# Kernel tuning notes

Measured on AMD Instinct MI355X. Metric: run time of the kernel, lower is better.

Reference implementation:

```python
import jax, jax.numpy as jnp
import numpy as np

D_MODEL = 128
NUM_HEADS = 4
HEAD_DIM = D_MODEL // NUM_HEADS  # 32
SCALE = 1.0 / np.sqrt(HEAD_DIM)
LAMBDA_INIT = 0.8
EPS = 1e-5


def _layernorm(x, w, b):
    mu = jnp.mean(x, axis=-1, keepdims=True)
    var = jnp.var(x, axis=-1, keepdims=True)
    return (x - mu) * jax.lax.rsqrt(var + EPS) * w + b


def setup_inputs() -> dict:
    key = jax.random.key(0)
    ks = jax.random.split(key, 10)
    B, T, D = 8, 2048, D_MODEL
    inp = {
        "tokens": jax.random.normal(ks[0], (B, T, D), dtype=jnp.float32),
        "ln_w": jnp.ones((D,), jnp.float32),
        "ln_b": jnp.zeros((D,), jnp.float32),
        "wq": jax.random.normal(ks[1], (D, 2 * D), jnp.float32) * (1.0 / np.sqrt(D)),
        "wk": jax.random.normal(ks[2], (D, 2 * D), jnp.float32) * (1.0 / np.sqrt(D)),
        "wv": jax.random.normal(ks[3], (D, 2 * D), jnp.float32) * (1.0 / np.sqrt(D)),
        "wo": jax.random.normal(ks[4], (2 * D, D), jnp.float32) * (1.0 / np.sqrt(2 * D)),
        "lambda_q1": jax.random.normal(ks[5], (HEAD_DIM,), jnp.float32) * 0.1,
        "lambda_k1": jax.random.normal(ks[6], (HEAD_DIM,), jnp.float32) * 0.1,
        "lambda_q2": jax.random.normal(ks[7], (HEAD_DIM,), jnp.float32) * 0.1,
        "lambda_k2": jax.random.normal(ks[8], (HEAD_DIM,), jnp.float32) * 0.1,
        "sigma_signal": jnp.asarray(3.0, jnp.float32),
        "sigma_noise": jnp.asarray(10.0, jnp.float32),
        "hn_w": jnp.ones((2 * HEAD_DIM,), jnp.float32),
        "hn_b": jnp.zeros((2 * HEAD_DIM,), jnp.float32),
    }
    return inp


def reference(tokens, ln_w, ln_b, wq, wk, wv, wo,
              lambda_q1, lambda_k1, lambda_q2, lambda_k2,
              sigma_signal, sigma_noise, hn_w, hn_b):
    B, T, D = tokens.shape
    H, hd = NUM_HEADS, HEAD_DIM

    x = _layernorm(tokens, ln_w, ln_b)

    def heads(x, w):  # [B,T,D] @ [D,2D] -> [B,H,T,2*hd]
        return (x @ w).reshape(B, T, H, 2 * hd).transpose(0, 2, 1, 3)

    q = heads(x, wq)
    k = heads(x, wk)
    v = heads(x, wv)
    q1, q2 = q[..., :hd], q[..., hd:]
    k1, k2 = k[..., :hd], k[..., hd:]

    scores1 = jnp.einsum('bhqd,bhkd->bhqk', q1, k1) * SCALE
    scores2 = jnp.einsum('bhqd,bhkd->bhqk', q2, k2) * SCALE

    # temporal Gaussian bias, shared sigma mode: [T,T] broadcast over [B,H]
    pos = jnp.arange(T, dtype=tokens.dtype)
    rel = pos[None, :] - pos[:, None]  # rel_dist[i,j] = j - i
    sig_s = jnp.maximum(sigma_signal, 1.0)
    sig_n = jnp.maximum(sigma_noise, 1.0)
    scores1 = scores1 + (-0.5 * (rel / sig_s) ** 2)
    scores2 = scores2 + (-0.5 * (rel / sig_n) ** 2)

    attn1 = jax.nn.softmax(scores1, axis=-1)
    attn2 = jax.nn.softmax(scores2, axis=-1)

    lam = jnp.exp(jnp.dot(lambda_q1, lambda_k1)) - jnp.exp(jnp.dot(lambda_q2, lambda_k2)) + LAMBDA_INIT

    out = jnp.einsum('bhqk,bhkd->bhqd', attn1 - lam * attn2, v)  # [B,H,T,2*hd]
    out = _layernorm(out, hn_w, hn_b)
    out = out * (1.0 - LAMBDA_INIT)
    out = out.transpose(0, 2, 1, 3).reshape(B, T, 2 * D)
    out = out @ wo
    return tokens + out
```

## Files before the change

### kernel.cpp

```cpp
#include <hip/hip_runtime.h>
#include <hip/hip_bf16.h>

#define TSEQ 2048
#define BATCH 8
#define NHEAD 4
#define BH (BATCH*NHEAD)
#define HD 32
#define SCALE 0.17677669529663687f
#define LAMBDA_INIT 0.8f
#define LN_EPS 1e-5f

typedef __attribute__((ext_vector_type(8))) short short8;
typedef __attribute__((ext_vector_type(4))) float f32x4;

static __device__ __forceinline__ unsigned short f2bf(float x) {
    unsigned int u = __float_as_uint(x);
    unsigned int r = (u + 0x7fffu + ((u >> 16) & 1u)) >> 16;
    return (unsigned short)r;
}

__global__ __launch_bounds__(256) void k_prep(
    const float* __restrict__ wq, const float* __restrict__ wk,
    const float* __restrict__ wv, const float* __restrict__ wo,
    unsigned short* __restrict__ WqkvT, unsigned short* __restrict__ WoT)
{
    __shared__ float xt[64][65];
    const int bid = blockIdx.x, tid = threadIdx.x;
    const float* src; int srcN, k0, nsrc0, dstK;
    unsigned short* dst;
    if (bid < 24) {
        int ntile = bid >> 1, ktile = bid & 1;
        int gn0 = ntile * 64; k0 = ktile * 64;
        int mat = gn0 >> 8;
        src = (mat == 0) ? wq : (mat == 1 ? wk : wv);
        srcN = 256; nsrc0 = gn0 & 255;
        dst = WqkvT + (size_t)gn0 * 128; dstK = 128;
    } else {
        int b2 = bid - 24;
        int ntile = b2 >> 2, ktile = b2 & 3;
        int gn0 = ntile * 64; k0 = ktile * 64;
        src = wo; srcN = 128; nsrc0 = gn0;
        dst = WoT + (size_t)gn0 * 256; dstK = 256;
    }
    {
        int r = tid >> 2, cs = tid & 3;
        const float* sp = src + (size_t)(k0 + r) * srcN + nsrc0 + cs * 16;
        #pragma unroll
        for (int j = 0; j < 4; j++) {
            float4 v = *(const float4*)(sp + j * 4);
            xt[r][cs * 16 + j * 4 + 0] = v.x;
            xt[r][cs * 16 + j * 4 + 1] = v.y;
            xt[r][cs * 16 + j * 4 + 2] = v.z;
            xt[r][cs * 16 + j * 4 + 3] = v.w;
        }
    }
    __syncthreads();
    {
        int n = tid >> 2, ks = tid & 3;
        short8 o0, o1;
        #pragma unroll
        for (int j = 0; j < 8; j++) {
            o0[j] = (short)f2bf(xt[ks * 16 + j][n]);
            o1[j] = (short)f2bf(xt[ks * 16 + 8 + j][n]);
        }
        unsigned short* dp = dst + (size_t)n * dstK + k0 + ks * 16;
        *(short8*)dp = o0;
        *(short8*)(dp + 8) = o1;
    }
}

__global__ __launch_bounds__(256) void k_qkv(
    const float* __restrict__ tokens, const float* __restrict__ ln_w,
    const float* __restrict__ ln_b, const unsigned short* __restrict__ WqkvT,
    unsigned short* __restrict__ Qg, unsigned short* __restrict__ Kg,
    unsigned short* __restrict__ Vtg)
{
    __shared__ unsigned short x_lds[32][132];
    __shared__ unsigned short c_lds[4][16][68];
    const int tid = threadIdx.x;
    const int r0 = blockIdx.x * 32;

    {
        int row = tid >> 3, sub = tid & 7;
        const float* tr = tokens + (size_t)(r0 + row) * 128 + sub * 16;
        float v[16]; float s = 0.f, sq = 0.f;
        #pragma unroll
        for (int j = 0; j < 16; j += 4) {
            float4 t4 = *(const float4*)(tr + j);
            v[j] = t4.x; v[j + 1] = t4.y; v[j + 2] = t4.z; v[j + 3] = t4.w;
        }
        #pragma unroll
        for (int j = 0; j < 16; j++) { s += v[j]; sq += v[j] * v[j]; }
        #pragma unroll
        for (int m = 1; m < 8; m <<= 1) { s += __shfl_xor(s, m, 64); sq += __shfl_xor(sq, m, 64); }
        float mean = s * (1.f / 128.f);
        float var  = sq * (1.f / 128.f) - mean * mean;
        float rstd = rsqrtf(var + LN_EPS);
        short8 o0, o1;
        #pragma unroll
        for (int j = 0; j < 8; j++) {
            int c0 = sub * 16 + j, c1 = sub * 16 + 8 + j;
            o0[j] = (short)f2bf((v[j] - mean) * rstd * ln_w[c0] + ln_b[c0]);
            o1[j] = (short)f2bf((v[8 + j] - mean) * rstd * ln_w[c1] + ln_b[c1]);
        }
        *(short8*)&x_lds[row][sub * 16] = o0;
        *(short8*)&x_lds[row][sub * 16 + 8] = o1;
    }
    __syncthreads();

    const int w = tid >> 6, lane = tid & 63;
    const int lg = lane >> 4, li = lane & 15;
    const int rt = w >> 1, ch = w & 1;

    short8 a[4];
    #pragma unroll
    for (int kc = 0; kc < 4; kc++)
        a[kc] = *(const short8*)&x_lds[rt * 16 + li][kc * 32 + lg * 8];

    const int b   = r0 >> 11;
    const int tw0 = (r0 & 2047) + rt * 16;

    #pragma unroll
    for (int cc = 0; cc < 6; cc++) {
        f32x4 acc[4] = {};
        #pragma unroll
        for (int t = 0; t < 4; t++) {
            int n0 = ch * 384 + cc * 64 + t * 16;
            const unsigned short* bp = WqkvT + (size_t)(n0 + li) * 128 + lg * 8;
            #pragma unroll
            for (int kc = 0; kc < 4; kc++) {
                short8 bf = *(const short8*)(bp + kc * 32);
                acc[t] = __builtin_amdgcn_mfma_f32_16x16x32_bf16(a[kc], bf, acc[t], 0, 0, 0);
            }
        }
        #pragma unroll
        for (int t = 0; t < 4; t++)
            #pragma unroll
            for (int r = 0; r < 4; r++)
                c_lds[w][lg * 4 + r][t * 16 + li] = f2bf(acc[t][r]);

        int gc = ch * 6 + cc;
        int kind = gc >> 2, h = gc & 3;
        size_t bhh = (size_t)(b * NHEAD + h);
        if (kind < 2) {
            unsigned short* base = (kind == 0) ? Qg : Kg;
            int row = lane >> 2, seg = lane & 3;
            unsigned short* dp = base + (bhh * TSEQ + tw0 + row) * 64 + seg * 16;
            *(short8*)dp       = *(const short8*)&c_lds[w][row][seg * 16];
            *(short8*)(dp + 8) = *(const short8*)&c_lds[w][row][seg * 16 + 8];
        } else {
            int d = lane;
            short8 v0, v1;
            #pragma unroll
            for (int j = 0; j < 8; j++) {
                v0[j] = (short)c_lds[w][j][d];
                v1[j] = (short)c_lds[w][8 + j][d];
            }
            unsigned short* dp = Vtg + (bhh * 64 + d) * TSEQ + tw0;
            *(short8*)dp = v0;
            *(short8*)(dp + 8) = v1;
        }
    }
}

__global__ __launch_bounds__(64) void k_attn(
    const unsigned short* __restrict__ Qg, const unsigned short* __restrict__ Kg,
    const unsigned short* __restrict__ Vtg,
    const float* __restrict__ lq1, const float* __restrict__ lk1,
    const float* __restrict__ lq2, const float* __restrict__ lk2,
    const float* __restrict__ sig_s_p, const float* __restrict__ sig_n_p,
    const float* __restrict__ hn_w, const float* __restrict__ hn_b,
    unsigned short* __restrict__ attn_out)
{
    __shared__ unsigned short p_lds[2][32][36];

    const int lane = threadIdx.x;
    const int lg   = lane >> 4;
    const int li   = lane & 15;

    const int xcd = blockIdx.x & 7;
    const int idx = blockIdx.x >> 3;
    const int bh  = (xcd << 2) | (idx >> 6);
    const int qw  = (idx & 63) * 32;

    float d1 = 0.f, d2 = 0.f;
    for (int i = 0; i < HD; i++) { d1 += lq1[i] * lk1[i]; d2 += lq2[i] * lk2[i]; }
    const float lam = __expf(d1) - __expf(d2) + LAMBDA_INIT;
    const float ss = fmaxf(sig_s_p[0], 1.f);
    const float sn = fmaxf(sig_n_p[0], 1.f);
    const float c1 = -0.5f / (ss * ss);
    const float c2 = -0.5f / (sn * sn);

    int W = (int)ceilf(fmaxf(ss, sn) * 8.f);
    W = (W + 31) & ~31;
    if (W < 64) W = 64;
    int lo = qw - W; if (lo < 0) lo = 0; lo &= ~31;
    int hi = qw + 32 + W; hi = (hi + 31) & ~31; if (hi > TSEQ) hi = TSEQ;

    short8 q1[2], q2[2];
    #pragma unroll
    for (int qt = 0; qt < 2; qt++) {
        const unsigned short* qp = Qg + ((size_t)bh * TSEQ + (qw + qt * 16 + li)) * 64;
        q1[qt] = *(const short8*)(qp + lg * 8);
        q2[qt] = *(const short8*)(qp + 32 + lg * 8);
    }

    const unsigned short* kbase = Kg  + ((size_t)bh * TSEQ + li) * 64 + lg * 8;
    const unsigned short* vbase = Vtg + ((size_t)bh * 64 + li) * TSEQ + lg * 8;

    f32x4 acc1[2][4] = {}, acc2[2][4] = {};
    float ls1[2][4] = {}, ls2[2][4] = {};
    const f32x4 zero4 = {0.f, 0.f, 0.f, 0.f};

    for (int kv = lo; kv < hi; kv += 32) {
        const unsigned short* kp = kbase + (size_t)kv * 64;
        short8 kf1[2], kf2[2];
        kf1[0] = *(const short8*)(kp);
        kf2[0] = *(const short8*)(kp + 32);
        kf1[1] = *(const short8*)(kp + 1024);
        kf2[1] = *(const short8*)(kp + 1024 + 32);

        #pragma unroll
        for (int qt = 0; qt < 2; qt++) {
            f32x4 s1[2], s2[2];
            #pragma unroll
            for (int kt = 0; kt < 2; kt++) {
                s1[kt] = __builtin_amdgcn_mfma_f32_16x16x32_bf16(q1[qt], kf1[kt], zero4, 0, 0, 0);
                s2[kt] = __builtin_amdgcn_mfma_f32_16x16x32_bf16(q2[qt], kf2[kt], zero4, 0, 0, 0);
            }
            const float rb = (float)(kv + li - qw - qt * 16 - 4 * lg);
            #pragma unroll
            for (int kt = 0; kt < 2; kt++) {
                #pragma unroll
                for (int r = 0; r < 4; r++) {
                    float rel = rb + (float)(16 * kt - r);
                    float rr  = rel * rel;
                    float e1  = __expf(fmaf(s1[kt][r], SCALE, c1 * rr));
                    float e2  = __expf(fmaf(s2[kt][r], SCALE, c2 * rr));
                    ls1[qt][r] += e1;
                    ls2[qt][r] += e2;
                    p_lds[0][qt * 16 + lg * 4 + r][kt * 16 + li] = f2bf(e1);
                    p_lds[1][qt * 16 + lg * 4 + r][kt * 16 + li] = f2bf(e2);
                }
            }
        }

        const unsigned short* vp = vbase + kv;
        short8 vf[4];
        #pragma unroll
        for (int dt = 0; dt < 4; dt++)
            vf[dt] = *(const short8*)(vp + (size_t)dt * 16 * TSEQ);

        #pragma unroll
        for (int qt = 0; qt < 2; qt++) {
            short8 pa1 = *(const short8*)&p_lds[0][qt * 16 + li][lg * 8];
            short8 pa2 = *(const short8*)&p_lds[1][qt * 16 + li][lg * 8];
            #pragma unroll
            for (int dt = 0; dt < 4; dt++) {
                acc1[qt][dt] = __builtin_amdgcn_mfma_f32_16x16x32_bf16(pa1, vf[dt], acc1[qt][dt], 0, 0, 0);
                acc2[qt][dt] = __builtin_amdgcn_mfma_f32_16x16x32_bf16(pa2, vf[dt], acc2[qt][dt], 0, 0, 0);
            }
        }
    }

    #pragma unroll
    for (int qt = 0; qt < 2; qt++)
        #pragma unroll
        for (int r = 0; r < 4; r++) {
            #pragma unroll
            for (int m = 1; m < 16; m <<= 1) {
                ls1[qt][r] += __shfl_xor(ls1[qt][r], m, 64);
                ls2[qt][r] += __shfl_xor(ls2[qt][r], m, 64);
            }
        }

    float hw[4], hb[4];
    #pragma unroll
    for (int t = 0; t < 4; t++) { hw[t] = hn_w[t * 16 + li]; hb[t] = hn_b[t * 16 + li]; }

    const int b = bh >> 2, h = bh & 3;
    #pragma unroll
    for (int qt = 0; qt < 2; qt++) {
        #pragma unroll
        for (int r = 0; r < 4; r++) {
            float il1 = 1.f / ls1[qt][r];
            float il2 = lam / ls2[qt][r];
            float o[4];
            float s = 0.f, sq = 0.f;
            #pragma unroll
            for (int t = 0; t < 4; t++) {
                o[t] = acc1[qt][t][r] * il1 - acc2[qt][t][r] * il2;
                s += o[t]; sq += o[t] * o[t];
            }
            #pragma unroll
            for (int m = 1; m < 16; m <<= 1) { s += __shfl_xor(s, m, 64); sq += __shfl_xor(sq, m, 64); }
            float mean = s * (1.f / 64.f);
            float var  = sq * (1.f / 64.f) - mean * mean;
            float rstd = rsqrtf(var + LN_EPS);
            int qrow = qw + qt * 16 + lg * 4 + r;
            unsigned short* op = attn_out + ((size_t)b * TSEQ + qrow) * 256 + h * 64;
            #pragma unroll
            for (int t = 0; t < 4; t++) {
                op[t * 16 + li] = f2bf(((o[t] - mean) * rstd * hw[t] + hb[t]) * 0.2f);
            }
        }
    }
}

__global__ __launch_bounds__(256) void k_out(
    const unsigned short* __restrict__ attn_out, const unsigned short* __restrict__ WoT,
    const float* __restrict__ tokens, float* __restrict__ out)
{
    const int tid = threadIdx.x;
    const int w = tid >> 6, lane = tid & 63;
    const int lg = lane >> 4, li = lane & 15;
    const int rt = w >> 1, chh = w & 1;
    const int r0 = blockIdx.x * 32 + rt * 16;

    short8 a[8];
    const unsigned short* ap = attn_out + (size_t)(r0 + li) * 256 + lg * 8;
    #pragma unroll
    for (int kc = 0; kc < 8; kc++) a[kc] = *(const short8*)(ap + kc * 32);

    #pragma unroll
    for (int c2 = 0; c2 < 4; c2++) {
        int ct = chh * 4 + c2;
        f32x4 acc = {};
        const unsigned short* bp = WoT + (size_t)(ct * 16 + li) * 256 + lg * 8;
        #pragma unroll
        for (int kc = 0; kc < 8; kc++) {
            short8 bf = *(const short8*)(bp + kc * 32);
            acc = __builtin_amdgcn_mfma_f32_16x16x32_bf16(a[kc], bf, acc, 0, 0, 0);
        }
        #pragma unroll
        for (int r = 0; r < 4; r++) {
            size_t idx = (size_t)(r0 + lg * 4 + r) * 128 + ct * 16 + li;
            out[idx] = tokens[idx] + acc[r];
        }
    }
}

extern "C" void kernel_launch(void* const* d_in, const int* in_sizes, int n_in,
                              void* d_out, int out_size, void* d_ws, size_t ws_size,
                              hipStream_t stream) {
    const float* tokens = (const float*)d_in[0];
    const float* ln_w   = (const float*)d_in[1];
    const float* ln_b   = (const float*)d_in[2];
    const float* wq     = (const float*)d_in[3];
    const float* wk     = (const float*)d_in[4];
    const float* wv     = (const float*)d_in[5];
    const float* wo     = (const float*)d_in[6];
    const float* lq1    = (const float*)d_in[7];
    const float* lk1    = (const float*)d_in[8];
    const float* lq2    = (const float*)d_in[9];
    const float* lk2    = (const float*)d_in[10];
    const float* sigs   = (const float*)d_in[11];
    const float* sign   = (const float*)d_in[12];
    const float* hn_w   = (const float*)d_in[13];
    const float* hn_b   = (const float*)d_in[14];

    const size_t n_qk = (size_t)BH * TSEQ * 64;
    unsigned short* Qg      = (unsigned short*)d_ws;
    unsigned short* Kg      = Qg + n_qk;
    unsigned short* Vtg     = Kg + n_qk;
    unsigned short* attn_o  = Vtg + n_qk;
    unsigned short* WqkvT   = attn_o + n_qk;
    unsigned short* WoT     = WqkvT + 768 * 128;

    k_prep<<<dim3(32), dim3(256), 0, stream>>>(wq, wk, wv, wo, WqkvT, WoT);
    k_qkv<<<dim3(BATCH * TSEQ / 32), dim3(256), 0, stream>>>(
        tokens, ln_w, ln_b, WqkvT, Qg, Kg, Vtg);
    k_attn<<<dim3(2048), dim3(64), 0, stream>>>(
        Qg, Kg, Vtg, lq1, lk1, lq2, lk2, sigs, sign, hn_w, hn_b, attn_o);
    k_out<<<dim3(BATCH * TSEQ / 32), dim3(256), 0, stream>>>(
        attn_o, WoT, tokens, (float*)d_out);
}
```

Measured before the change: 74.02 us.

## Fuse attention and output projection into one kernel with per-head waves

Merges the attention kernel and the output-projection kernel into a single 256-thread block. Each of the four waves handles one head for the same 32-query tile, and the normalized head outputs are staged in LDS. After a block barrier, the Wo matmul and residual add run from that LDS tile. This removes the bf16 attention-output round trip through global memory and one kernel launch, at the cost of fewer, larger blocks (512 instead of 2048), more LDS per block, and a barrier that ties the four head waves together.

```diff
diff --git a/kernel.cpp b/kernel.cpp
--- a/kernel.cpp
+++ b/kernel.cpp
@@ -163,25 +163,28 @@
     }
 }
 
-__global__ __launch_bounds__(64) void k_attn(
+__global__ __launch_bounds__(256) void k_attn2(
     const unsigned short* __restrict__ Qg, const unsigned short* __restrict__ Kg,
     const unsigned short* __restrict__ Vtg,
     const float* __restrict__ lq1, const float* __restrict__ lk1,
     const float* __restrict__ lq2, const float* __restrict__ lk2,
     const float* __restrict__ sig_s_p, const float* __restrict__ sig_n_p,
     const float* __restrict__ hn_w, const float* __restrict__ hn_b,
-    unsigned short* __restrict__ attn_out)
+    const unsigned short* __restrict__ WoT, const float* __restrict__ tokens,
+    float* __restrict__ out)
 {
-    __shared__ unsigned short p_lds[2][32][36];
-
-    const int lane = threadIdx.x;
+    __shared__ unsigned short p_lds[4][2][32][36];
+    __shared__ unsigned short ao[32][264];
+
+    const int tid  = threadIdx.x;
+    const int w    = tid >> 6;
+    const int lane = tid & 63;
     const int lg   = lane >> 4;
     const int li   = lane & 15;
 
-    const int xcd = blockIdx.x & 7;
-    const int idx = blockIdx.x >> 3;
-    const int bh  = (xcd << 2) | (idx >> 6);
-    const int qw  = (idx & 63) * 32;
+    const int b  = blockIdx.x & 7;
+    const int qw = (blockIdx.x >> 3) * 32;
+    const int bh = b * NHEAD + w;
 
     float d1 = 0.f, d2 = 0.f;
     for (int i = 0; i < HD; i++) { d1 += lq1[i] * lk1[i]; d2 += lq2[i] * lk2[i]; }
@@ -239,8 +242,8 @@
                     float e2  = __expf(fmaf(s2[kt][r], SCALE, c2 * rr));
                     ls1[qt][r] += e1;
                     ls2[qt][r] += e2;
-                    p_lds[0][qt * 16 + lg * 4 + r][kt * 16 + li] = f2bf(e1);
-                    p_lds[1][qt * 16 + lg * 4 + r][kt * 16 + li] = f2bf(e2);
+                    p_lds[w][0][qt * 16 + lg * 4 + r][kt * 16 + li] = f2bf(e1);
+                    p_lds[w][1][qt * 16 + lg * 4 + r][kt * 16 + li] = f2bf(e2);
                 }
             }
         }
@@ -253,8 +256,8 @@
 
         #pragma unroll
         for (int qt = 0; qt < 2; qt++) {
-            short8 pa1 = *(const short8*)&p_lds[0][qt * 16 + li][lg * 8];
-            short8 pa2 = *(const short8*)&p_lds[1][qt * 16 + li][lg * 8];
+            short8 pa1 = *(const short8*)&p_lds[w][0][qt * 16 + li][lg * 8];
+            short8 pa2 = *(const short8*)&p_lds[w][1][qt * 16 + li][lg * 8];
             #pragma unroll
             for (int dt = 0; dt < 4; dt++) {
                 acc1[qt][dt] = __builtin_amdgcn_mfma_f32_16x16x32_bf16(pa1, vf[dt], acc1[qt][dt], 0, 0, 0);
@@ -274,68 +277,62 @@
             }
         }
 
-    float hw[4], hb[4];
-    #pragma unroll
-    for (int t = 0; t < 4; t++) { hw[t] = hn_w[t * 16 + li]; hb[t] = hn_b[t * 16 + li]; }
-
-    const int b = bh >> 2, h = bh & 3;
-    #pragma unroll
-    for (int qt = 0; qt < 2; qt++) {
-        #pragma unroll
-        for (int r = 0; r < 4; r++) {
-            float il1 = 1.f / ls1[qt][r];
-            float il2 = lam / ls2[qt][r];
-            float o[4];
-            float s = 0.f, sq = 0.f;
-            #pragma unroll
-            for (int t = 0; t < 4; t++) {
-                o[t] = acc1[qt][t][r] * il1 - acc2[qt][t][r] * il2;
-                s += o[t]; sq += o[t] * o[t];
-            }
-            #pragma unroll
-            for (int m = 1; m < 16; m <<= 1) { s += __shfl_xor(s, m, 64); sq += __shfl_xor(sq, m, 64); }
-            float mean = s * (1.f / 64.f);
-            float var  = sq * (1.f / 64.f) - mean * mean;
-            float rstd = rsqrtf(var + LN_EPS);
-            int qrow = qw + qt * 16 + lg * 4 + r;
-            unsigned short* op = attn_out + ((size_t)b * TSEQ + qrow) * 256 + h * 64;
-            #pragma unroll
-            for (int t = 0; t < 4; t++) {
-                op[t * 16 + li] = f2bf(((o[t] - mean) * rstd * hw[t] + hb[t]) * 0.2f);
-            }
-        }
-    }
-}
-
-__global__ __launch_bounds__(256) void k_out(
-    const unsigned short* __restrict__ attn_out, const unsigned short* __restrict__ WoT,
-    const float* __restrict__ tokens, float* __restrict__ out)
-{
-    const int tid = threadIdx.x;
-    const int w = tid >> 6, lane = tid & 63;
-    const int lg = lane >> 4, li = lane & 15;
-    const int rt = w >> 1, chh = w & 1;
-    const int r0 = blockIdx.x * 32 + rt * 16;
-
-    short8 a[8];
-    const unsigned short* ap = attn_out + (size_t)(r0 + li) * 256 + lg * 8;
-    #pragma unroll
-    for (int kc = 0; kc < 8; kc++) a[kc] = *(const short8*)(ap + kc * 32);
-
-    #pragma unroll
-    for (int c2 = 0; c2 < 4; c2++) {
-        int ct = chh * 4 + c2;
-        f32x4 acc = {};
+    {
+        float hw[4], hb[4];
+        #pragma unroll
+        for (int t = 0; t < 4; t++) { hw[t] = hn_w[t * 16 + li]; hb[t] = hn_b[t * 16 + li]; }
+
+        #pragma unroll
+        for (int qt = 0; qt < 2; qt++) {
+            #pragma unroll
+            for (int r = 0; r < 4; r++) {
+                float il1 = 1.f / ls1[qt][r];
+                float il2 = lam / ls2[qt][r];
+                float o[4];
+                float s = 0.f, sq = 0.f;
+                #pragma unroll
+                for (int t = 0; t < 4; t++) {
+                    o[t] = acc1[qt][t][r] * il1 - acc2[qt][t][r] * il2;
+                    s += o[t]; sq += o[t] * o[t];
+                }
+                #pragma unroll
+                for (int m = 1; m < 16; m <<= 1) { s += __shfl_xor(s, m, 64); sq += __shfl_xor(sq, m, 64); }
+                float mean = s * (1.f / 64.f);
+                float var  = sq * (1.f / 64.f) - mean * mean;
+                float rstd = rsqrtf(var + LN_EPS);
+                int arow = qt * 16 + lg * 4 + r;
+                #pragma unroll
+                for (int t = 0; t < 4; t++) {
+                    ao[arow][w * 64 + t * 16 + li] =
+                        f2bf(((o[t] - mean) * rstd * hw[t] + hb[t]) * 0.2f);
+                }
+            }
+        }
+    }
+    __syncthreads();
+
+    const int row0 = b * TSEQ + qw;
+    #pragma unroll
+    for (int c2 = 0; c2 < 2; c2++) {
+        const int ct = w * 2 + c2;
+        short8 bfr[8];
         const unsigned short* bp = WoT + (size_t)(ct * 16 + li) * 256 + lg * 8;
         #pragma unroll
-        for (int kc = 0; kc < 8; kc++) {
-            short8 bf = *(const short8*)(bp + kc * 32);
-            acc = __builtin_amdgcn_mfma_f32_16x16x32_bf16(a[kc], bf, acc, 0, 0, 0);
-        }
-        #pragma unroll
-        for (int r = 0; r < 4; r++) {
-            size_t idx = (size_t)(r0 + lg * 4 + r) * 128 + ct * 16 + li;
-            out[idx] = tokens[idx] + acc[r];
+        for (int kc = 0; kc < 8; kc++) bfr[kc] = *(const short8*)(bp + kc * 32);
+
+        #pragma unroll
+        for (int qt = 0; qt < 2; qt++) {
+            f32x4 acc = {};
+            #pragma unroll
+            for (int kc = 0; kc < 8; kc++) {
+                short8 af = *(const short8*)&ao[qt * 16 + li][kc * 32 + lg * 8];
+                acc = __builtin_amdgcn_mfma_f32_16x16x32_bf16(af, bfr[kc], acc, 0, 0, 0);
+            }
+            #pragma unroll
+            for (int r = 0; r < 4; r++) {
+                size_t idx = (size_t)(row0 + qt * 16 + lg * 4 + r) * 128 + ct * 16 + li;
+                out[idx] = tokens[idx] + acc[r];
+            }
         }
     }
 }
@@ -363,15 +360,13 @@
     unsigned short* Qg      = (unsigned short*)d_ws;
     unsigned short* Kg      = Qg + n_qk;
     unsigned short* Vtg     = Kg + n_qk;
-    unsigned short* attn_o  = Vtg + n_qk;
-    unsigned short* WqkvT   = attn_o + n_qk;
+    unsigned short* WqkvT   = Vtg + n_qk;
     unsigned short* WoT     = WqkvT + 768 * 128;
 
     k_prep<<<dim3(32), dim3(256), 0, stream>>>(wq, wk, wv, wo, WqkvT, WoT);
     k_qkv<<<dim3(BATCH * TSEQ / 32), dim3(256), 0, stream>>>(
         tokens, ln_w, ln_b, WqkvT, Qg, Kg, Vtg);
-    k_attn<<<dim3(2048), dim3(64), 0, stream>>>(
-        Qg, Kg, Vtg, lq1, lk1, lq2, lk2, sigs, sign, hn_w, hn_b, attn_o);
-    k_out<<<dim3(BATCH * TSEQ / 32), dim3(256), 0, stream>>>(
-        attn_o, WoT, tokens, (float*)d_out);
-}
+    k_attn2<<<dim3(512), dim3(256), 0, stream>>>(
+        Qg, Kg, Vtg, lq1, lk1, lq2, lk2, sigs, sign, hn_w, hn_b,
+        WoT, tokens, (float*)d_out);
+}
```

New measurement: 65.34 us. 11.7% less time.
